# Kernel tuning notes

Measured on AMD Instinct MI355X. Metric: run time of the kernel, lower is better.

## Reference

```python
import jax, jax.numpy as jnp
import numpy as np

B, T, V, E, U = 64, 4995, 4096, 100, 64


def gru_layer(x, W, R, b, return_sequences):
    """Keras GRU (reset_after=True). x: [B,T,D]. Returns [B,T,U] or [B,U]."""
    u = R.shape[0]
    # Precompute all input projections in one big matmul: [B,T,3u]
    xp = jnp.einsum('btd,dk->btk', x, W) + b[0]
    h0 = jnp.zeros((x.shape[0], u), dtype=x.dtype)

    def step(h, xt):
        hp = h @ R + b[1]                                   # [B,3u]
        z = jax.nn.sigmoid(xt[:, :u] + hp[:, :u])
        r = jax.nn.sigmoid(xt[:, u:2 * u] + hp[:, u:2 * u])
        hh = jnp.tanh(xt[:, 2 * u:] + r * hp[:, 2 * u:])
        h_new = z * h + (1.0 - z) * hh
        return h_new, (h_new if return_sequences else None)

    hT, ys = jax.lax.scan(step, h0, jnp.swapaxes(xp, 0, 1))  # scan over time
    if return_sequences:
        return jnp.swapaxes(ys, 0, 1)                        # [B,T,U]
    return hT                                                # [B,U]


def setup_inputs() -> dict:
    key = jax.random.key(0)
    ks = jax.random.split(key, 8)
    s = 0.05
    return {
        'tokens': jax.random.randint(ks[0], (B, T), 0, V, dtype=jnp.int32),
        'emb': jax.random.normal(ks[1], (V, E), jnp.float32) * s,
        'W1': jax.random.normal(ks[2], (E, 3 * U), jnp.float32) * s,
        'U1': jax.random.normal(ks[3], (U, 3 * U), jnp.float32) * s,
        'b1': jnp.zeros((2, 3 * U), jnp.float32),
        'W2': jax.random.normal(ks[4], (U, 3 * U), jnp.float32) * s,
        'U2': jax.random.normal(ks[5], (U, 3 * U), jnp.float32) * s,
        'b2': jnp.zeros((2, 3 * U), jnp.float32),
        'Wout': jax.random.normal(ks[6], (U, 1), jnp.float32) * s,
        'bout': jnp.zeros((1,), jnp.float32),
    }


def reference(tokens, emb, W1, U1, b1, W2, U2, b2, Wout, bout):
    x = emb[tokens]                                   # [B,T,E] embedding lookup
    x = gru_layer(x, W1, U1, b1, return_sequences=True)   # [B,T,U]
    h = gru_layer(x, W2, U2, b2, return_sequences=False)  # [B,U] (last state)
    logits = h @ Wout + bout                          # [B,1]
    return jax.nn.sigmoid(logits)
```

## Files before the change

kernel.cpp:

```cpp
#include <hip/hip_runtime.h>

#define BB 64
#define TT 4995
#define VV 4096
#define EE 100
#define UU 64
#define U3 192
#define BPB 4
#define NBLK (BB / BPB)

using bf16x8 = __attribute__((ext_vector_type(8))) short;
using f32x4  = __attribute__((ext_vector_type(4))) float;

#define MFMA16 __builtin_amdgcn_mfma_f32_16x16x32_bf16

__device__ float g_embW[VV * U3];

__device__ __forceinline__ float fast_sigmoid(float x) {
    return __builtin_amdgcn_rcpf(1.0f + __expf(-x));
}
__device__ __forceinline__ float fast_tanh(float x) {
    return __builtin_amdgcn_rcpf(1.0f + __expf(-2.0f * x)) * 2.0f - 1.0f;
}
__device__ __forceinline__ unsigned short f2bf(float f) {
    unsigned u = __float_as_uint(f);
    return (unsigned short)((u + 0x7FFFu + ((u >> 16) & 1u)) >> 16);
}
__device__ __forceinline__ float bf2f(unsigned short h) {
    return __uint_as_float(((unsigned)h) << 16);
}

__global__ void gru_embw_kernel(const float* __restrict__ emb,
                                const float* __restrict__ W1,
                                const float* __restrict__ b1) {
    __shared__ float row[EE];
    const int v = blockIdx.x;
    const int k = threadIdx.x;
    if (k < EE) row[k] = emb[v * EE + k];
    __syncthreads();
    float acc = b1[k];
    #pragma unroll 4
    for (int j = 0; j < EE; ++j)
        acc = fmaf(row[j], W1[j * U3 + k], acc);
    g_embW[v * U3 + k] = acc;
}

__global__ __launch_bounds__(512, 1)
void gru_scan_kernel(const int* __restrict__ tokens,
                     const float* __restrict__ U1,
                     const float* __restrict__ b1,
                     const float* __restrict__ W2,
                     const float* __restrict__ U2,
                     const float* __restrict__ b2,
                     const float* __restrict__ Wout,
                     const float* __restrict__ bout,
                     float* __restrict__ out) {
    const int blk  = blockIdx.x;
    const int tid  = threadIdx.x;
    const int wave = tid >> 6;
    const int lane = tid & 63;
    const int lg   = lane >> 4;
    const int lc   = lane & 15;
    const bool isL2 = (wave >= 4);
    const int ut   = wave & 3;

    __shared__ __align__(16) char hls[8192];
    for (int i = tid; i < 2048; i += 512) ((int*)hls)[i] = 0;

    bf16x8 fb[12];
    const int cz = ut * 16 + lc;
    const int cr = 64 + ut * 16 + lc;
    const int ch = 128 + ut * 16 + lc;
    {
        const float* M0 = isL2 ? W2 : U1;
        #pragma unroll
        for (int g = 0; g < 3; ++g) {
            const int col = g * 64 + ut * 16 + lc;
            #pragma unroll
            for (int kk = 0; kk < 2; ++kk) {
                bf16x8 v;
                #pragma unroll
                for (int e = 0; e < 8; ++e)
                    v[e] = (short)f2bf(M0[(8 * lg + 32 * kk + e) * U3 + col]);
                fb[g * 2 + kk] = v;
            }
        }
        if (isL2) {
            #pragma unroll
            for (int g = 0; g < 3; ++g) {
                const int col = g * 64 + ut * 16 + lc;
                #pragma unroll
                for (int kk = 0; kk < 2; ++kk) {
                    bf16x8 v;
                    #pragma unroll
                    for (int e = 0; e < 8; ++e)
                        v[e] = (short)f2bf(U2[(8 * lg + 32 * kk + e) * U3 + col]);
                    fb[6 + g * 2 + kk] = v;
                }
            }
        } else {
            #pragma unroll
            for (int q = 6; q < 12; ++q) fb[q] = fb[q - 6];
        }
    }

    float bias_z, bias_r, bias_h, bias_h2 = 0.0f;
    if (!isL2) {
        bias_z = b1[U3 + cz]; bias_r = b1[U3 + cr]; bias_h = b1[U3 + ch];
    } else {
        bias_z  = b2[cz] + b2[U3 + cz];
        bias_r  = b2[cr] + b2[U3 + cr];
        bias_h  = b2[ch];
        bias_h2 = b2[U3 + ch];
    }

    float xp[2][3];
    int   tok[2];
    const int rowbase = (blk * BPB + lg) * TT;
    if (!isL2) {
        const int t0 = tokens[rowbase];
        tok[0] = tokens[rowbase + 1];
        tok[1] = tokens[rowbase + 2];
        xp[0][0] = g_embW[t0 * U3 + cz];
        xp[0][1] = g_embW[t0 * U3 + cr];
        xp[0][2] = g_embW[t0 * U3 + ch];
    }

    float h1o = 0.0f;
    float h2o = 0.0f;

    __syncthreads();

    const int swzA = (lc & 7) << 4;
    const int myrow = 4 * lg;
    const int wswz  = ((myrow & 7) << 4);
    const int wbyte = myrow * 128 + (((ut * 16 + lc) * 2) ^ wswz);

    #pragma unroll 1
    for (int sb = 0; sb < TT + 1; sb += 2) {
        #pragma unroll
        for (int half = 0; half < 2; ++half) {
            const int s = sb + half;
            char* rdb = hls + half * 4096;
            char* wrb = hls + (half ^ 1) * 4096;

            bf16x8 a1_0 = *(const bf16x8*)(rdb + lc * 128 + ((16 * lg) ^ swzA));
            bf16x8 a1_1 = *(const bf16x8*)(rdb + lc * 128 + ((16 * lg + 64) ^ swzA));
            bf16x8 a2_0 = *(const bf16x8*)(rdb + 2048 + lc * 128 + ((16 * lg) ^ swzA));
            bf16x8 a2_1 = *(const bf16x8*)(rdb + 2048 + lc * 128 + ((16 * lg + 64) ^ swzA));

            if (!isL2) {
                const int tn = tok[half];
                xp[half ^ 1][0] = g_embW[tn * U3 + cz];
                xp[half ^ 1][1] = g_embW[tn * U3 + cr];
                xp[half ^ 1][2] = g_embW[tn * U3 + ch];
                const int s2 = (s + 2 < TT) ? (s + 2) : (TT - 1);
                tok[half ^ 1] = tokens[rowbase + s2];

                if (s < TT) {
                    f32x4 az = {bias_z, bias_z, bias_z, bias_z};
                    f32x4 ar = {bias_r, bias_r, bias_r, bias_r};
                    f32x4 ah = {bias_h, bias_h, bias_h, bias_h};
                    az = MFMA16(a1_0, fb[0], az, 0, 0, 0);
                    az = MFMA16(a1_1, fb[1], az, 0, 0, 0);
                    ar = MFMA16(a1_0, fb[2], ar, 0, 0, 0);
                    ar = MFMA16(a1_1, fb[3], ar, 0, 0, 0);
                    ah = MFMA16(a1_0, fb[4], ah, 0, 0, 0);
                    ah = MFMA16(a1_1, fb[5], ah, 0, 0, 0);
                    const float z  = fast_sigmoid(xp[half][0] + az[0]);
                    const float rg = fast_sigmoid(xp[half][1] + ar[0]);
                    const float hh = fast_tanh(xp[half][2] + rg * ah[0]);
                    h1o = z * h1o + (1.0f - z) * hh;
                    *(unsigned short*)(wrb + wbyte) = f2bf(h1o);
                }
            } else {
                if (s > 0) {
                    f32x4 az = {bias_z,  bias_z,  bias_z,  bias_z };
                    f32x4 ar = {bias_r,  bias_r,  bias_r,  bias_r };
                    f32x4 ax = {bias_h,  bias_h,  bias_h,  bias_h };
                    f32x4 ap = {bias_h2, bias_h2, bias_h2, bias_h2};
                    az = MFMA16(a1_0, fb[0],  az, 0, 0, 0);
                    az = MFMA16(a1_1, fb[1],  az, 0, 0, 0);
                    az = MFMA16(a2_0, fb[6],  az, 0, 0, 0);
                    az = MFMA16(a2_1, fb[7],  az, 0, 0, 0);
                    ar = MFMA16(a1_0, fb[2],  ar, 0, 0, 0);
                    ar = MFMA16(a1_1, fb[3],  ar, 0, 0, 0);
                    ar = MFMA16(a2_0, fb[8],  ar, 0, 0, 0);
                    ar = MFMA16(a2_1, fb[9],  ar, 0, 0, 0);
                    ax = MFMA16(a1_0, fb[4],  ax, 0, 0, 0);
                    ax = MFMA16(a1_1, fb[5],  ax, 0, 0, 0);
                    ap = MFMA16(a2_0, fb[10], ap, 0, 0, 0);
                    ap = MFMA16(a2_1, fb[11], ap, 0, 0, 0);
                    const float z  = fast_sigmoid(az[0]);
                    const float rg = fast_sigmoid(ar[0]);
                    const float hh = fast_tanh(ax[0] + rg * ap[0]);
                    h2o = z * h2o + (1.0f - z) * hh;
                    *(unsigned short*)(wrb + 2048 + wbyte) = f2bf(h2o);
                }
            }
            __syncthreads();
        }
    }

    if (wave == 0 && lane < BPB) {
        const int row = 4 * lane;
        float acc = bout[0];
        #pragma unroll 8
        for (int u = 0; u < UU; ++u) {
            const unsigned short hv = *(const unsigned short*)(hls + 2048 +
                row * 128 + ((u * 2) ^ ((row & 7) << 4)));
            acc = fmaf(bf2f(hv), Wout[u], acc);
        }
        out[blk * BPB + lane] = fast_sigmoid(acc);
    }
}

extern "C" void kernel_launch(void* const* d_in, const int* in_sizes, int n_in,
                              void* d_out, int out_size, void* d_ws, size_t ws_size,
                              hipStream_t stream) {
    const int*   tokens = (const int*)  d_in[0];
    const float* emb    = (const float*)d_in[1];
    const float* W1     = (const float*)d_in[2];
    const float* U1w    = (const float*)d_in[3];
    const float* b1     = (const float*)d_in[4];
    const float* W2     = (const float*)d_in[5];
    const float* U2w    = (const float*)d_in[6];
    const float* b2     = (const float*)d_in[7];
    const float* Wout   = (const float*)d_in[8];
    const float* bout   = (const float*)d_in[9];
    float* out = (float*)d_out;

    gru_embw_kernel<<<VV, 192, 0, stream>>>(emb, W1, b1);
    gru_scan_kernel<<<NBLK, 512, 0, stream>>>(tokens, U1w, b1, W2, U2w,
                                              b2, Wout, bout, out);
}
```

Measured before the change: 1.612 ms.

## Break MFMA accumulation chains, load only needed LDS operands, lighter barrier

Each gate's dependent MFMA accumulation chain is split into independent MFMAs whose results are summed on the VALU. This shortens the serial latency on the recurrent critical path. LDS operand loads move into each layer branch, so layer-1 waves no longer read layer-2 state. __syncthreads is replaced with an inline-asm lgkmcnt wait plus s_barrier. The changes add a few extra adds and slightly change the floating-point summation order.

```diff
diff --git a/kernel.cpp b/kernel.cpp
--- a/kernel.cpp
+++ b/kernel.cpp
@@ -13,6 +13,8 @@
 using f32x4  = __attribute__((ext_vector_type(4))) float;
 
 #define MFMA16 __builtin_amdgcn_mfma_f32_16x16x32_bf16
+
+#define LDS_BARRIER() asm volatile("s_waitcnt lgkmcnt(0)\ns_barrier" ::: "memory")
 
 __device__ float g_embW[VV * U3];
 
@@ -113,6 +115,11 @@
         bias_h  = b2[ch];
         bias_h2 = b2[U3 + ch];
     }
+    const f32x4 bz4 = {bias_z, bias_z, bias_z, bias_z};
+    const f32x4 br4 = {bias_r, bias_r, bias_r, bias_r};
+    const f32x4 bh4 = {bias_h, bias_h, bias_h, bias_h};
+    const f32x4 bp4 = {bias_h2, bias_h2, bias_h2, bias_h2};
+    const f32x4 zq  = {0.0f, 0.0f, 0.0f, 0.0f};
 
     float xp[2][3];
     int   tok[2];
@@ -144,12 +151,10 @@
             char* rdb = hls + half * 4096;
             char* wrb = hls + (half ^ 1) * 4096;
 
-            bf16x8 a1_0 = *(const bf16x8*)(rdb + lc * 128 + ((16 * lg) ^ swzA));
-            bf16x8 a1_1 = *(const bf16x8*)(rdb + lc * 128 + ((16 * lg + 64) ^ swzA));
-            bf16x8 a2_0 = *(const bf16x8*)(rdb + 2048 + lc * 128 + ((16 * lg) ^ swzA));
-            bf16x8 a2_1 = *(const bf16x8*)(rdb + 2048 + lc * 128 + ((16 * lg + 64) ^ swzA));
-
             if (!isL2) {
+                bf16x8 a1_0 = *(const bf16x8*)(rdb + lc * 128 + ((16 * lg) ^ swzA));
+                bf16x8 a1_1 = *(const bf16x8*)(rdb + lc * 128 + ((16 * lg + 64) ^ swzA));
+
                 const int tn = tok[half];
                 xp[half ^ 1][0] = g_embW[tn * U3 + cz];
                 xp[half ^ 1][1] = g_embW[tn * U3 + cr];
@@ -158,47 +163,47 @@
                 tok[half ^ 1] = tokens[rowbase + s2];
 
                 if (s < TT) {
-                    f32x4 az = {bias_z, bias_z, bias_z, bias_z};
-                    f32x4 ar = {bias_r, bias_r, bias_r, bias_r};
-                    f32x4 ah = {bias_h, bias_h, bias_h, bias_h};
-                    az = MFMA16(a1_0, fb[0], az, 0, 0, 0);
-                    az = MFMA16(a1_1, fb[1], az, 0, 0, 0);
-                    ar = MFMA16(a1_0, fb[2], ar, 0, 0, 0);
-                    ar = MFMA16(a1_1, fb[3], ar, 0, 0, 0);
-                    ah = MFMA16(a1_0, fb[4], ah, 0, 0, 0);
-                    ah = MFMA16(a1_1, fb[5], ah, 0, 0, 0);
-                    const float z  = fast_sigmoid(xp[half][0] + az[0]);
-                    const float rg = fast_sigmoid(xp[half][1] + ar[0]);
-                    const float hh = fast_tanh(xp[half][2] + rg * ah[0]);
+                    const f32x4 azA = MFMA16(a1_0, fb[0], bz4, 0, 0, 0);
+                    const f32x4 azB = MFMA16(a1_1, fb[1], zq,  0, 0, 0);
+                    const f32x4 arA = MFMA16(a1_0, fb[2], br4, 0, 0, 0);
+                    const f32x4 arB = MFMA16(a1_1, fb[3], zq,  0, 0, 0);
+                    const f32x4 ahA = MFMA16(a1_0, fb[4], bh4, 0, 0, 0);
+                    const f32x4 ahB = MFMA16(a1_1, fb[5], zq,  0, 0, 0);
+                    const float z  = fast_sigmoid(xp[half][0] + (azA[0] + azB[0]));
+                    const float rg = fast_sigmoid(xp[half][1] + (arA[0] + arB[0]));
+                    const float hh = fast_tanh(xp[half][2] + rg * (ahA[0] + ahB[0]));
                     h1o = z * h1o + (1.0f - z) * hh;
                     *(unsigned short*)(wrb + wbyte) = f2bf(h1o);
                 }
             } else {
+                bf16x8 a1_0 = *(const bf16x8*)(rdb + lc * 128 + ((16 * lg) ^ swzA));
+                bf16x8 a1_1 = *(const bf16x8*)(rdb + lc * 128 + ((16 * lg + 64) ^ swzA));
+                bf16x8 a2_0 = *(const bf16x8*)(rdb + 2048 + lc * 128 + ((16 * lg) ^ swzA));
+                bf16x8 a2_1 = *(const bf16x8*)(rdb + 2048 + lc * 128 + ((16 * lg + 64) ^ swzA));
+
                 if (s > 0) {
-                    f32x4 az = {bias_z,  bias_z,  bias_z,  bias_z };
-                    f32x4 ar = {bias_r,  bias_r,  bias_r,  bias_r };
-                    f32x4 ax = {bias_h,  bias_h,  bias_h,  bias_h };
-                    f32x4 ap = {bias_h2, bias_h2, bias_h2, bias_h2};
-                    az = MFMA16(a1_0, fb[0],  az, 0, 0, 0);
-                    az = MFMA16(a1_1, fb[1],  az, 0, 0, 0);
-                    az = MFMA16(a2_0, fb[6],  az, 0, 0, 0);
-                    az = MFMA16(a2_1, fb[7],  az, 0, 0, 0);
-                    ar = MFMA16(a1_0, fb[2],  ar, 0, 0, 0);
-                    ar = MFMA16(a1_1, fb[3],  ar, 0, 0, 0);
-                    ar = MFMA16(a2_0, fb[8],  ar, 0, 0, 0);
-                    ar = MFMA16(a2_1, fb[9],  ar, 0, 0, 0);
-                    ax = MFMA16(a1_0, fb[4],  ax, 0, 0, 0);
-                    ax = MFMA16(a1_1, fb[5],  ax, 0, 0, 0);
-                    ap = MFMA16(a2_0, fb[10], ap, 0, 0, 0);
-                    ap = MFMA16(a2_1, fb[11], ap, 0, 0, 0);
-                    const float z  = fast_sigmoid(az[0]);
-                    const float rg = fast_sigmoid(ar[0]);
-                    const float hh = fast_tanh(ax[0] + rg * ap[0]);
+                    const f32x4 azA = MFMA16(a1_0, fb[0],  bz4, 0, 0, 0);
+                    const f32x4 azB = MFMA16(a1_1, fb[1],  zq,  0, 0, 0);
+                    const f32x4 azC = MFMA16(a2_0, fb[6],  zq,  0, 0, 0);
+                    const f32x4 azD = MFMA16(a2_1, fb[7],  zq,  0, 0, 0);
+                    const f32x4 arA = MFMA16(a1_0, fb[2],  br4, 0, 0, 0);
+                    const f32x4 arB = MFMA16(a1_1, fb[3],  zq,  0, 0, 0);
+                    const f32x4 arC = MFMA16(a2_0, fb[8],  zq,  0, 0, 0);
+                    const f32x4 arD = MFMA16(a2_1, fb[9],  zq,  0, 0, 0);
+                    const f32x4 axA = MFMA16(a1_0, fb[4],  bh4, 0, 0, 0);
+                    const f32x4 axB = MFMA16(a1_1, fb[5],  zq,  0, 0, 0);
+                    const f32x4 apA = MFMA16(a2_0, fb[10], bp4, 0, 0, 0);
+                    const f32x4 apB = MFMA16(a2_1, fb[11], zq,  0, 0, 0);
+                    const float zs = (azA[0] + azB[0]) + (azC[0] + azD[0]);
+                    const float rs = (arA[0] + arB[0]) + (arC[0] + arD[0]);
+                    const float z  = fast_sigmoid(zs);
+                    const float rg = fast_sigmoid(rs);
+                    const float hh = fast_tanh((axA[0] + axB[0]) + rg * (apA[0] + apB[0]));
                     h2o = z * h2o + (1.0f - z) * hh;
                     *(unsigned short*)(wrb + 2048 + wbyte) = f2bf(h2o);
                 }
             }
-            __syncthreads();
+            LDS_BARRIER();
         }
     }
 
```

New measurement: 1.992 ms. +23.5%, slower.
